# Kernel optimization log

Measured on AMD Instinct MI355X. Metric: run time of the kernel, lower is better.

## Reference

```python
import jax, jax.numpy as jnp
import numpy as np

M = 16        # multiheads
D = 64        # head_dim
ODIM = M * D  # 1024, input feature dim
B = 64        # raw batch (divisible by M)
L = 512       # sequence length
X = B // M    # folded batch after the view trick
NEG = 1.0e12
SCALE = float(1.0 / np.sqrt(D))


def _proj(x, w, b):
    # x: [B, L, ODIM] -> linear to [B, L, D] -> fold batch -> [X, M, L, D]
    y = x @ w.T + b                    # [B, L, D]
    y = y.reshape(-1, L, M, D)         # [X, L, M, D] (row-major, == torch .view)
    return y.transpose(0, 2, 1, 3)     # [X, M, L, D]


def setup_inputs() -> dict:
    key = jax.random.key(0)
    ks = jax.random.split(key, 12)
    f32 = jnp.float32
    inp = {
        "Q_seq": jax.random.normal(ks[0], (B, L, ODIM), f32),
        "K_seq": jax.random.normal(ks[1], (B, L, ODIM), f32),
        "V_seq": jax.random.normal(ks[2], (B, L, ODIM), f32),
        "Q_len": jax.random.randint(ks[3], (X, 1), 1, L),
        "V_len": jax.random.randint(ks[4], (X, 1), 1, L),
        "WQ_w": jax.random.normal(ks[5], (D, ODIM), f32) * 0.02,
        "WQ_b": jnp.zeros((D,), f32),
        "WK_w": jax.random.normal(ks[6], (D, ODIM), f32) * 0.02,
        "WK_b": jnp.zeros((D,), f32),
        "WV_w": jax.random.normal(ks[7], (D, ODIM), f32) * 0.02,
        "WV_b": jnp.zeros((D,), f32),
    }
    return inp


def reference(Q_seq, K_seq, V_seq, Q_len, V_len, WQ_w, WQ_b, WK_w, WK_b, WV_w, WV_b):
    Q = _proj(Q_seq, WQ_w, WQ_b)   # [X, M, L, D]
    K = _proj(K_seq, WK_w, WK_b)
    V = _proj(V_seq, WV_w, WV_b)

    A = jnp.einsum("xmqd,xmkd->xmqk", Q, K) * SCALE   # [X, M, Lq, Lk]

    # key-length (V_len) padding mask: valid where position < V_len
    key_valid = (jnp.arange(L) < V_len[:, :1]).astype(A.dtype)   # [X, Lk]
    A = A - (1.0 - key_valid)[:, None, None, :] * NEG

    # causal mask (mask_right=True)
    causal = jnp.triu(jnp.ones((L, L), A.dtype), k=1) * NEG
    A = A - causal

    A = jax.nn.softmax(A, axis=-1)
    O = jnp.einsum("xmqk,xmkd->xmqd", A, V)            # [X, M, L, D]
    O = O.transpose(0, 2, 1, 3).reshape(-1, L, M * D)  # [X, L, ODIM]

    # query-length (Q_len) multiplicative mask
    q_valid = (jnp.arange(L) < Q_len[:, :1]).astype(O.dtype)     # [X, L]
    return O * q_valid[:, :, None]
```

## Files before the change

kernel.cpp:

```cpp
#include <hip/hip_runtime.h>


typedef _Float16 half8 __attribute__((ext_vector_type(8)));
typedef _Float16 half4v __attribute__((ext_vector_type(4)));
typedef float f32x4 __attribute__((ext_vector_type(4)));

#define LSEQ 512
#define ODIM 1024
#define NG   64
#define HD   64
#define GSTRIDE ((size_t)LSEQ * HD)
#define TSIZE  ((size_t)NG * LSEQ * HD)

__global__ __launch_bounds__(256) void proj_kernel(
    const float* __restrict__ Qs, const float* __restrict__ Ks,
    const float* __restrict__ Vs,
    const float* __restrict__ WQ, const float* __restrict__ bQ,
    const float* __restrict__ WK, const float* __restrict__ bK,
    const float* __restrict__ WV, const float* __restrict__ bV,
    _Float16* __restrict__ ws)
{
    const int p = blockIdx.y;
    const float* in; const float* W; const float* bias;
    if (p == 0)      { in = Qs; W = WQ; bias = bQ; }
    else if (p == 1) { in = Ks; W = WK; bias = bK; }
    else             { in = Vs; W = WV; bias = bV; }
    _Float16* outp = ws + (size_t)p * TSIZE;

    __shared__ _Float16 lds[9216];
    _Float16* Al = lds;
    _Float16* Wl = lds + 128 * 40;
    _Float16* Cl = lds;

    const int t    = threadIdx.x;
    const int lane = t & 63;
    const int w    = t >> 6;
    const int quad = lane >> 4;
    const int c    = lane & 15;

    const size_t rowBase = (size_t)blockIdx.x * 128;
    const float* Ag = in + rowBase * ODIM;

    f32x4 acc[2][4];
    #pragma unroll
    for (int i = 0; i < 2; ++i)
        #pragma unroll
        for (int j = 0; j < 4; ++j) { f32x4 z = {0.f,0.f,0.f,0.f}; acc[i][j] = z; }

    const int rr = t >> 3;
    const int c4 = (t & 7) * 4;

    for (int kt = 0; kt < 32; ++kt) {
        __syncthreads();
        #pragma unroll
        for (int j = 0; j < 4; ++j) {
            int row = j * 32 + rr;
            float4 v = *(const float4*)(Ag + (size_t)row * ODIM + kt * 32 + c4);
            half4v h; h[0] = (_Float16)v.x; h[1] = (_Float16)v.y;
                      h[2] = (_Float16)v.z; h[3] = (_Float16)v.w;
            *(half4v*)&Al[row * 40 + c4] = h;
        }
        #pragma unroll
        for (int j = 0; j < 2; ++j) {
            int row = j * 32 + rr;
            float4 v = *(const float4*)(W + (size_t)row * ODIM + kt * 32 + c4);
            half4v h; h[0] = (_Float16)v.x; h[1] = (_Float16)v.y;
                      h[2] = (_Float16)v.z; h[3] = (_Float16)v.w;
            *(half4v*)&Wl[row * 40 + c4] = h;
        }
        __syncthreads();

        half8 a0 = *(const half8*)&Al[(w * 32 + c) * 40 + quad * 8];
        half8 a1 = *(const half8*)&Al[(w * 32 + 16 + c) * 40 + quad * 8];
        #pragma unroll
        for (int ct = 0; ct < 4; ++ct) {
            half8 b = *(const half8*)&Wl[(ct * 16 + c) * 40 + quad * 8];
            acc[0][ct] = __builtin_amdgcn_mfma_f32_16x16x32_f16(a0, b, acc[0][ct], 0, 0, 0);
            acc[1][ct] = __builtin_amdgcn_mfma_f32_16x16x32_f16(a1, b, acc[1][ct], 0, 0, 0);
        }
    }

    float bv[4];
    #pragma unroll
    for (int ct = 0; ct < 4; ++ct) bv[ct] = bias[ct * 16 + c];

    __syncthreads();
    #pragma unroll
    for (int rt = 0; rt < 2; ++rt)
        #pragma unroll
        for (int ct = 0; ct < 4; ++ct)
            #pragma unroll
            for (int r = 0; r < 4; ++r)
                Cl[(w * 32 + rt * 16 + quad * 4 + r) * 72 + ct * 16 + c] =
                    (_Float16)(acc[rt][ct][r] + bv[ct]);
    __syncthreads();

    const int chunk = t & 7;
    #pragma unroll
    for (int j = 0; j < 4; ++j) {
        int row = j * 32 + rr;
        int n   = (int)rowBase + row;
        int b_i = n >> 9;
        int l   = n & 511;
        int g   = ((b_i >> 4) << 4) + (l & 15);
        int l2  = ((b_i & 15) << 5) + (l >> 4);
        half8 v = *(const half8*)&Cl[row * 72 + chunk * 8];
        *(half8*)(outp + ((size_t)g * LSEQ + l2) * HD + chunk * 8) = v;
    }
}

__global__ __launch_bounds__(256) void attn_kernel(
    const _Float16* __restrict__ ws, const int* __restrict__ Qlen,
    const int* __restrict__ Vlen, float* __restrict__ out)
{
    const _Float16* Qws = ws;
    const _Float16* Kws = ws + TSIZE;
    const _Float16* Vws = ws + 2 * TSIZE;

    const int qt = blockIdx.x;
    const int g  = blockIdx.y;
    const int x  = g >> 4;
    const int m  = g & 15;
    const int qlen = Qlen[x];
    const int vlen = Vlen[x];
    const int q0 = qt * 64;

    const int t    = threadIdx.x;
    const int lane = t & 63;
    const int w    = t >> 6;
    const int quad = lane >> 4;
    const int c    = lane & 15;

    if (q0 >= qlen) {
        int row = t >> 2, d0 = (t & 3) * 16;
        float4 z = make_float4(0.f, 0.f, 0.f, 0.f);
        float* dst = out + ((size_t)(x * LSEQ + q0 + row)) * ODIM + m * 64 + d0;
        #pragma unroll
        for (int j = 0; j < 4; ++j) *(float4*)(dst + j * 4) = z;
        return;
    }

    __shared__ _Float16 Ql[64 * 72];
    __shared__ _Float16 Kl[64 * 72];
    __shared__ _Float16 Vt[64 * 72];
    __shared__ _Float16 Pl[4][16 * 72];

    {
        int row = t >> 2, d0 = (t & 3) * 16;
        const _Float16* src = Qws + ((size_t)g * LSEQ + q0 + row) * HD + d0;
        *(half8*)&Ql[row * 72 + d0]     = *(const half8*)src;
        *(half8*)&Ql[row * 72 + d0 + 8] = *(const half8*)(src + 8);
    }
    __syncthreads();
    const half8 aq0 = *(const half8*)&Ql[(w * 16 + c) * 72 + quad * 8];
    const half8 aq1 = *(const half8*)&Ql[(w * 16 + c) * 72 + 32 + quad * 8];

    f32x4 o[4];
    #pragma unroll
    for (int i = 0; i < 4; ++i) { f32x4 z = {0.f,0.f,0.f,0.f}; o[i] = z; }
    float mO[4], lO[4];
    #pragma unroll
    for (int r = 0; r < 4; ++r) { mO[r] = -1e30f; lO[r] = 0.f; }
    const int qrow_base = q0 + w * 16 + quad * 4;

    for (int kt = 0; kt <= qt; ++kt) {
        __syncthreads();
        {
            int row = t >> 2, d0 = (t & 3) * 16;
            const _Float16* ksrc = Kws + ((size_t)g * LSEQ + kt * 64 + row) * HD + d0;
            *(half8*)&Kl[row * 72 + d0]     = *(const half8*)ksrc;
            *(half8*)&Kl[row * 72 + d0 + 8] = *(const half8*)(ksrc + 8);
            const _Float16* vsrc = Vws + ((size_t)g * LSEQ + kt * 64 + row) * HD + d0;
            half8 v0 = *(const half8*)vsrc;
            half8 v1 = *(const half8*)(vsrc + 8);
            #pragma unroll
            for (int j = 0; j < 8; ++j) {
                Vt[(d0 + j) * 72 + row]     = v0[j];
                Vt[(d0 + 8 + j) * 72 + row] = v1[j];
            }
        }
        __syncthreads();

        f32x4 s[4];
        #pragma unroll
        for (int ct = 0; ct < 4; ++ct) {
            half8 b0 = *(const half8*)&Kl[(ct * 16 + c) * 72 + quad * 8];
            half8 b1 = *(const half8*)&Kl[(ct * 16 + c) * 72 + 32 + quad * 8];
            f32x4 z = {0.f,0.f,0.f,0.f};
            z = __builtin_amdgcn_mfma_f32_16x16x32_f16(aq0, b0, z, 0, 0, 0);
            z = __builtin_amdgcn_mfma_f32_16x16x32_f16(aq1, b1, z, 0, 0, 0);
            s[ct] = z;
        }

        #pragma unroll
        for (int ct = 0; ct < 4; ++ct) {
            int kcol = kt * 64 + ct * 16 + c;
            #pragma unroll
            for (int r = 0; r < 4; ++r) {
                int qr = qrow_base + r;
                float sv = s[ct][r] * 0.125f;
                s[ct][r] = (kcol <= qr && kcol < vlen) ? sv : -1e30f;
            }
        }

        #pragma unroll
        for (int r = 0; r < 4; ++r) {
            float v = fmaxf(fmaxf(s[0][r], s[1][r]), fmaxf(s[2][r], s[3][r]));
            v = fmaxf(v, __shfl_xor(v, 1, 64));
            v = fmaxf(v, __shfl_xor(v, 2, 64));
            v = fmaxf(v, __shfl_xor(v, 4, 64));
            v = fmaxf(v, __shfl_xor(v, 8, 64));
            float mn = fmaxf(mO[r], v);
            float alpha = __expf(mO[r] - mn);
            mO[r] = mn;
            float rs = 0.f;
            #pragma unroll
            for (int ct = 0; ct < 4; ++ct) {
                float pv = __expf(s[ct][r] - mn);
                s[ct][r] = pv;
                rs += pv;
            }
            rs += __shfl_xor(rs, 1, 64);
            rs += __shfl_xor(rs, 2, 64);
            rs += __shfl_xor(rs, 4, 64);
            rs += __shfl_xor(rs, 8, 64);
            lO[r] = lO[r] * alpha + rs;
            #pragma unroll
            for (int dct = 0; dct < 4; ++dct) o[dct][r] *= alpha;
        }

        #pragma unroll
        for (int ct = 0; ct < 4; ++ct)
            #pragma unroll
            for (int r = 0; r < 4; ++r)
                Pl[w][(quad * 4 + r) * 72 + ct * 16 + c] = (_Float16)s[ct][r];

        half8 pa0 = *(const half8*)&Pl[w][c * 72 + quad * 8];
        half8 pa1 = *(const half8*)&Pl[w][c * 72 + 32 + quad * 8];
        #pragma unroll
        for (int dct = 0; dct < 4; ++dct) {
            half8 vb0 = *(const half8*)&Vt[(dct * 16 + c) * 72 + quad * 8];
            half8 vb1 = *(const half8*)&Vt[(dct * 16 + c) * 72 + 32 + quad * 8];
            o[dct] = __builtin_amdgcn_mfma_f32_16x16x32_f16(pa0, vb0, o[dct], 0, 0, 0);
            o[dct] = __builtin_amdgcn_mfma_f32_16x16x32_f16(pa1, vb1, o[dct], 0, 0, 0);
        }
    }

    #pragma unroll
    for (int r = 0; r < 4; ++r) {
        int qr = qrow_base + r;
        float f = (qr < qlen) ? (1.0f / lO[r]) : 0.0f;
        #pragma unroll
        for (int dct = 0; dct < 4; ++dct)
            out[((size_t)(x * LSEQ + qr)) * ODIM + m * 64 + dct * 16 + c] =
                o[dct][r] * f;
    }
}

extern "C" void kernel_launch(void* const* d_in, const int* in_sizes, int n_in,
                              void* d_out, int out_size, void* d_ws, size_t ws_size,
                              hipStream_t stream) {
    const float* Qs  = (const float*)d_in[0];
    const float* Ks  = (const float*)d_in[1];
    const float* Vs  = (const float*)d_in[2];
    const int* Qlen  = (const int*)d_in[3];
    const int* Vlen  = (const int*)d_in[4];
    const float* WQ  = (const float*)d_in[5];
    const float* bQ  = (const float*)d_in[6];
    const float* WK  = (const float*)d_in[7];
    const float* bK  = (const float*)d_in[8];
    const float* WV  = (const float*)d_in[9];
    const float* bV  = (const float*)d_in[10];
    float* out = (float*)d_out;
    _Float16* ws = (_Float16*)d_ws;

    proj_kernel<<<dim3(256, 3), 256, 0, stream>>>(Qs, Ks, Vs, WQ, bQ, WK, bK, WV, bV, ws);
    attn_kernel<<<dim3(8, 64), 256, 0, stream>>>(ws, Qlen, Vlen, out);
}
```

Before: 408.8 us.

## Double-buffer projection GEMM, pre-transpose V in workspace, rotate attention tiles

The projection kernel now uses 64-row tiles with twice as many blocks, and its K-loop is register-prefetched and double-buffered in LDS, so global loads overlap with MFMA work and one barrier per step is dropped. The V projection writes its output already transposed into per-64-key tiles, which removes the scalar LDS transpose from the attention inner loop. Attention blocks rotate their query-tile index by the group index to spread causal work more evenly across the grid. Risks are the extra LDS footprint and less reuse of each W tile per block.

```diff
diff --git a/kernel.cpp b/kernel.cpp
--- a/kernel.cpp
+++ b/kernel.cpp
@@ -9,7 +9,6 @@
 #define ODIM 1024
 #define NG   64
 #define HD   64
-#define GSTRIDE ((size_t)LSEQ * HD)
 #define TSIZE  ((size_t)NG * LSEQ * HD)
 
 __global__ __launch_bounds__(256) void proj_kernel(
@@ -27,10 +26,7 @@
     else             { in = Vs; W = WV; bias = bV; }
     _Float16* outp = ws + (size_t)p * TSIZE;
 
-    __shared__ _Float16 lds[9216];
-    _Float16* Al = lds;
-    _Float16* Wl = lds + 128 * 40;
-    _Float16* Cl = lds;
+    __shared__ _Float16 lds[10240];
 
     const int t    = threadIdx.x;
     const int lane = t & 63;
@@ -38,74 +34,101 @@
     const int quad = lane >> 4;
     const int c    = lane & 15;
 
-    const size_t rowBase = (size_t)blockIdx.x * 128;
+    const size_t rowBase = (size_t)blockIdx.x * 64;
     const float* Ag = in + rowBase * ODIM;
-
-    f32x4 acc[2][4];
-    #pragma unroll
-    for (int i = 0; i < 2; ++i)
-        #pragma unroll
-        for (int j = 0; j < 4; ++j) { f32x4 z = {0.f,0.f,0.f,0.f}; acc[i][j] = z; }
-
     const int rr = t >> 3;
     const int c4 = (t & 7) * 4;
 
+    float4 pa0, pa1, pw0, pw1;
+
+#define LOADT(kt) do { \
+    pa0 = *(const float4*)(Ag + (size_t)rr        * ODIM + (kt) * 32 + c4); \
+    pa1 = *(const float4*)(Ag + (size_t)(rr + 32) * ODIM + (kt) * 32 + c4); \
+    pw0 = *(const float4*)(W  + (size_t)rr        * ODIM + (kt) * 32 + c4); \
+    pw1 = *(const float4*)(W  + (size_t)(rr + 32) * ODIM + (kt) * 32 + c4); \
+} while (0)
+
+#define STORET(buf) do { \
+    _Float16* Al_ = lds + (buf) * 5120; _Float16* Wl_ = Al_ + 2560; \
+    half4v h; \
+    h[0]=(_Float16)pa0.x; h[1]=(_Float16)pa0.y; h[2]=(_Float16)pa0.z; h[3]=(_Float16)pa0.w; \
+    *(half4v*)&Al_[rr * 40 + c4] = h; \
+    h[0]=(_Float16)pa1.x; h[1]=(_Float16)pa1.y; h[2]=(_Float16)pa1.z; h[3]=(_Float16)pa1.w; \
+    *(half4v*)&Al_[(rr + 32) * 40 + c4] = h; \
+    h[0]=(_Float16)pw0.x; h[1]=(_Float16)pw0.y; h[2]=(_Float16)pw0.z; h[3]=(_Float16)pw0.w; \
+    *(half4v*)&Wl_[rr * 40 + c4] = h; \
+    h[0]=(_Float16)pw1.x; h[1]=(_Float16)pw1.y; h[2]=(_Float16)pw1.z; h[3]=(_Float16)pw1.w; \
+    *(half4v*)&Wl_[(rr + 32) * 40 + c4] = h; \
+} while (0)
+
+    LOADT(0); STORET(0);
+    LOADT(1);
+
+    f32x4 acc[4];
+    #pragma unroll
+    for (int j = 0; j < 4; ++j) { f32x4 z = {0.f,0.f,0.f,0.f}; acc[j] = z; }
+
     for (int kt = 0; kt < 32; ++kt) {
         __syncthreads();
-        #pragma unroll
-        for (int j = 0; j < 4; ++j) {
-            int row = j * 32 + rr;
-            float4 v = *(const float4*)(Ag + (size_t)row * ODIM + kt * 32 + c4);
-            half4v h; h[0] = (_Float16)v.x; h[1] = (_Float16)v.y;
-                      h[2] = (_Float16)v.z; h[3] = (_Float16)v.w;
-            *(half4v*)&Al[row * 40 + c4] = h;
-        }
-        #pragma unroll
-        for (int j = 0; j < 2; ++j) {
-            int row = j * 32 + rr;
-            float4 v = *(const float4*)(W + (size_t)row * ODIM + kt * 32 + c4);
-            half4v h; h[0] = (_Float16)v.x; h[1] = (_Float16)v.y;
-                      h[2] = (_Float16)v.z; h[3] = (_Float16)v.w;
-            *(half4v*)&Wl[row * 40 + c4] = h;
-        }
-        __syncthreads();
-
-        half8 a0 = *(const half8*)&Al[(w * 32 + c) * 40 + quad * 8];
-        half8 a1 = *(const half8*)&Al[(w * 32 + 16 + c) * 40 + quad * 8];
-        #pragma unroll
-        for (int ct = 0; ct < 4; ++ct) {
-            half8 b = *(const half8*)&Wl[(ct * 16 + c) * 40 + quad * 8];
-            acc[0][ct] = __builtin_amdgcn_mfma_f32_16x16x32_f16(a0, b, acc[0][ct], 0, 0, 0);
-            acc[1][ct] = __builtin_amdgcn_mfma_f32_16x16x32_f16(a1, b, acc[1][ct], 0, 0, 0);
-        }
-    }
+        const _Float16* Al = lds + (kt & 1) * 5120;
+        const _Float16* Wl = Al + 2560;
+        half8 a  = *(const half8*)&Al[(w * 16 + c) * 40 + quad * 8];
+        half8 b0 = *(const half8*)&Wl[(0 * 16 + c) * 40 + quad * 8];
+        half8 b1 = *(const half8*)&Wl[(1 * 16 + c) * 40 + quad * 8];
+        half8 b2 = *(const half8*)&Wl[(2 * 16 + c) * 40 + quad * 8];
+        half8 b3 = *(const half8*)&Wl[(3 * 16 + c) * 40 + quad * 8];
+        if (kt < 31) STORET((kt + 1) & 1);
+        if (kt < 30) LOADT(kt + 2);
+        acc[0] = __builtin_amdgcn_mfma_f32_16x16x32_f16(a, b0, acc[0], 0, 0, 0);
+        acc[1] = __builtin_amdgcn_mfma_f32_16x16x32_f16(a, b1, acc[1], 0, 0, 0);
+        acc[2] = __builtin_amdgcn_mfma_f32_16x16x32_f16(a, b2, acc[2], 0, 0, 0);
+        acc[3] = __builtin_amdgcn_mfma_f32_16x16x32_f16(a, b3, acc[3], 0, 0, 0);
+    }
+#undef LOADT
+#undef STORET
 
     float bv[4];
     #pragma unroll
     for (int ct = 0; ct < 4; ++ct) bv[ct] = bias[ct * 16 + c];
 
+    _Float16* Cl = lds;
+    #pragma unroll
+    for (int ct = 0; ct < 4; ++ct)
+        #pragma unroll
+        for (int r = 0; r < 4; ++r)
+            Cl[(w * 16 + quad * 4 + r) * 72 + ct * 16 + c] =
+                (_Float16)(acc[ct][r] + bv[ct]);
     __syncthreads();
-    #pragma unroll
-    for (int rt = 0; rt < 2; ++rt)
-        #pragma unroll
-        for (int ct = 0; ct < 4; ++ct)
-            #pragma unroll
-            for (int r = 0; r < 4; ++r)
-                Cl[(w * 32 + rt * 16 + quad * 4 + r) * 72 + ct * 16 + c] =
-                    (_Float16)(acc[rt][ct][r] + bv[ct]);
-    __syncthreads();
-
-    const int chunk = t & 7;
-    #pragma unroll
-    for (int j = 0; j < 4; ++j) {
-        int row = j * 32 + rr;
-        int n   = (int)rowBase + row;
-        int b_i = n >> 9;
-        int l   = n & 511;
+
+    const int b_i = (int)(rowBase >> 9);
+    const int l0  = (int)(rowBase & 511);
+
+    if (p < 2) {
+        int row = t >> 2;
+        int chunk = t & 3;
+        int l   = l0 + row;
         int g   = ((b_i >> 4) << 4) + (l & 15);
         int l2  = ((b_i & 15) << 5) + (l >> 4);
-        half8 v = *(const half8*)&Cl[row * 72 + chunk * 8];
-        *(half8*)(outp + ((size_t)g * LSEQ + l2) * HD + chunk * 8) = v;
+        _Float16* dst = outp + ((size_t)g * LSEQ + l2) * HD;
+        *(half8*)(dst + chunk * 8)       = *(const half8*)&Cl[row * 72 + chunk * 8];
+        *(half8*)(dst + (chunk + 4) * 8) = *(const half8*)&Cl[row * 72 + (chunk + 4) * 8];
+    } else {
+        int d  = t & 63;
+        int gi = t >> 6;
+        int g_base = (b_i >> 4) << 4;
+        int l2_0   = ((b_i & 15) << 5) + (l0 >> 4);
+        int kt2 = l2_0 >> 6;
+        int kk  = l2_0 & 63;
+        #pragma unroll
+        for (int i = 0; i < 4; ++i) {
+            int g_idx = i * 4 + gi;
+            half4v v;
+            #pragma unroll
+            for (int j = 0; j < 4; ++j)
+                v[j] = Cl[(g_idx + 16 * j) * 72 + d];
+            size_t off = (((size_t)(g_base + g_idx) * 8 + kt2) * 64 + d) * 64 + kk;
+            *(half4v*)(outp + off) = v;
+        }
     }
 }
 
@@ -117,7 +140,7 @@
     const _Float16* Kws = ws + TSIZE;
     const _Float16* Vws = ws + 2 * TSIZE;
 
-    const int qt = blockIdx.x;
+    const int qt = (blockIdx.x + blockIdx.y) & 7;
     const int g  = blockIdx.y;
     const int x  = g >> 4;
     const int m  = g & 15;
@@ -170,14 +193,9 @@
             const _Float16* ksrc = Kws + ((size_t)g * LSEQ + kt * 64 + row) * HD + d0;
             *(half8*)&Kl[row * 72 + d0]     = *(const half8*)ksrc;
             *(half8*)&Kl[row * 72 + d0 + 8] = *(const half8*)(ksrc + 8);
-            const _Float16* vsrc = Vws + ((size_t)g * LSEQ + kt * 64 + row) * HD + d0;
-            half8 v0 = *(const half8*)vsrc;
-            half8 v1 = *(const half8*)(vsrc + 8);
-            #pragma unroll
-            for (int j = 0; j < 8; ++j) {
-                Vt[(d0 + j) * 72 + row]     = v0[j];
-                Vt[(d0 + 8 + j) * 72 + row] = v1[j];
-            }
+            const _Float16* vsrc = Vws + (((size_t)g * 8 + kt) * 64 + row) * 64 + d0;
+            *(half8*)&Vt[row * 72 + d0]     = *(const half8*)vsrc;
+            *(half8*)&Vt[row * 72 + d0 + 8] = *(const half8*)(vsrc + 8);
         }
         __syncthreads();
 
@@ -274,6 +292,6 @@
     float* out = (float*)d_out;
     _Float16* ws = (_Float16*)d_ws;
 
-    proj_kernel<<<dim3(256, 3), 256, 0, stream>>>(Qs, Ks, Vs, WQ, bQ, WK, bK, WV, bV, ws);
+    proj_kernel<<<dim3(512, 3), 256, 0, stream>>>(Qs, Ks, Vs, WQ, bQ, WK, bK, WV, bV, ws);
     attn_kernel<<<dim3(8, 64), 256, 0, stream>>>(ws, Qlen, Vlen, out);
 }
```

Result: slower. 417.8 us (+2.2%).
